# Performance work log

Hardware: AMD Instinct MI355X
Metric: run time of the kernel (lower is better)

## Reference

```python
import jax, jax.numpy as jnp
import numpy as np

B, L, C = 4, 2048, 512
D_STATE, D_CONV, EXPAND = 16, 4, 2
D_INNER = EXPAND * C
DT_RANK = C // 16  # mamba_ssm 'auto' dt_rank


def setup_inputs() -> dict:
    key = jax.random.key(0)
    ks = jax.random.split(key, 12)
    s = 0.02
    p = {}
    p["x"] = jax.random.normal(ks[0], (B, L, C), jnp.float32)
    p["gamma1"] = jnp.ones((C,), jnp.float32)
    p["beta1"] = jnp.zeros((C,), jnp.float32)
    # leading dim 2 = (forward mamba, backward mamba)
    p["W_in"] = jax.random.normal(ks[1], (2, 2 * D_INNER, C), jnp.float32) * s
    p["conv_w"] = jax.random.normal(ks[2], (2, D_INNER, D_CONV), jnp.float32) * s
    p["conv_b"] = jnp.zeros((2, D_INNER), jnp.float32)
    p["W_xproj"] = jax.random.normal(ks[3], (2, DT_RANK + 2 * D_STATE, D_INNER), jnp.float32) * s
    p["W_dt"] = jax.random.normal(ks[4], (2, D_INNER, DT_RANK), jnp.float32) * s
    p["b_dt"] = jax.random.normal(ks[5], (2, D_INNER), jnp.float32) * s
    p["A_log"] = jnp.tile(jnp.log(jnp.arange(1, D_STATE + 1, dtype=jnp.float32))[None, None, :], (2, D_INNER, 1))
    p["Dp"] = jnp.ones((2, D_INNER), jnp.float32)
    p["W_out"] = jax.random.normal(ks[6], (2, C, D_INNER), jnp.float32) * s
    p["gamma2"] = jnp.ones((C,), jnp.float32)
    p["beta2"] = jnp.zeros((C,), jnp.float32)
    p["W1"] = jax.random.normal(ks[7], (4 * C, C), jnp.float32) * s
    p["b1"] = jnp.zeros((4 * C,), jnp.float32)
    p["W2"] = jax.random.normal(ks[8], (C, 4 * C), jnp.float32) * s
    p["b2"] = jnp.zeros((C,), jnp.float32)
    return p


def layer_norm(x, g, b, eps=1e-5):
    mu = x.mean(-1, keepdims=True)
    var = ((x - mu) ** 2).mean(-1, keepdims=True)
    return (x - mu) * jax.lax.rsqrt(var + eps) * g + b


def mamba_one(x, W_in, conv_w, conv_b, W_xproj, W_dt, b_dt, A_log, Dv, W_out):
    # x: [B, L, C] -> [B, L, C]; faithful to mamba_ssm Mamba (in_proj no bias,
    # depthwise causal conv1d with bias, x_proj no bias, dt_proj with bias, out_proj no bias)
    u, z = jnp.split(x @ W_in.T, 2, axis=-1)          # [B,L,d_inner] each
    uc = jnp.pad(u.transpose(0, 2, 1), ((0, 0), (0, 0), (D_CONV - 1, 0)))  # causal pad
    uc = jax.lax.conv_general_dilated(uc, conv_w[:, None, :], (1,), 'VALID',
                                      feature_group_count=D_INNER)
    u = jax.nn.silu((uc + conv_b[None, :, None]).transpose(0, 2, 1))       # [B,L,d_inner]
    x_dbl = u @ W_xproj.T                              # [B,L,dt_rank+2*d_state]
    dt = jax.nn.softplus(x_dbl[..., :DT_RANK] @ W_dt.T + b_dt)             # [B,L,d_inner]
    Bm = x_dbl[..., DT_RANK:DT_RANK + D_STATE]         # [B,L,d_state]
    Cm = x_dbl[..., DT_RANK + D_STATE:]                # [B,L,d_state]
    A = -jnp.exp(A_log)                                # [d_inner,d_state]

    def step(h, ins):
        dt_t, B_t, C_t, u_t = ins                      # [B,d],[B,s],[B,s],[B,d]
        h = jnp.exp(dt_t[..., None] * A) * h + (dt_t * u_t)[..., None] * B_t[:, None, :]
        return h, jnp.einsum('bds,bs->bd', h, C_t)

    h0 = jnp.zeros((x.shape[0], D_INNER, D_STATE), x.dtype)
    xs = (dt.transpose(1, 0, 2), Bm.transpose(1, 0, 2), Cm.transpose(1, 0, 2), u.transpose(1, 0, 2))
    _, ys = jax.lax.scan(step, h0, xs)                 # ys: [L,B,d_inner]
    y = ys.transpose(1, 0, 2) + u * Dv
    y = y * jax.nn.silu(z)
    return y @ W_out.T


def reference(x, gamma1, beta1, W_in, conv_w, conv_b, W_xproj, W_dt, b_dt,
              A_log, Dp, W_out, gamma2, beta2, W1, b1, W2, b2):
    xn = layer_norm(x, gamma1, beta1)
    x2 = jnp.stack([xn, jnp.flip(xn, axis=1)])         # [2,B,L,C]
    ys = jax.vmap(mamba_one)(x2, W_in, conv_w, conv_b, W_xproj, W_dt, b_dt, A_log, Dp, W_out)
    y = (ys[0] + jnp.flip(ys[1], axis=1)) * 0.5
    x = x + y                                          # residual (dropout=0)
    h = jax.nn.gelu(layer_norm(x, gamma2, beta2) @ W1.T + b1, approximate=False)
    return x + (h @ W2.T + b2)
```

## Files before the change

### kernel.cpp

```cpp
#include <hip/hip_runtime.h>
#include <math.h>

#define B_ 4
#define L_ 2048
#define C_ 512
#define DI 1024
#define DS 16
#define NTOK 8192
#define SLICE ((long)NTOK * DI)
#define T_ 64
#define NC_ 32
#define SDT_LD 264

typedef __attribute__((ext_vector_type(4))) float  f32x4;
typedef __attribute__((ext_vector_type(4))) short  s16x4;
typedef __attribute__((ext_vector_type(8))) short  s16x8;
typedef __attribute__((ext_vector_type(8))) __bf16 bf16x8;

#define LOG2E 1.4426950408889634f
#define LN2   0.69314718055994531f

__device__ __forceinline__ float bf2f(short s) {
  return __uint_as_float(((unsigned)(unsigned short)s) << 16);
}
__device__ __forceinline__ short f2bf(float f) {
  return __builtin_bit_cast(short, (__bf16)f);
}
__device__ __forceinline__ f32x4 mfma16(s16x8 a, s16x8 b, f32x4 c) {
  return __builtin_amdgcn_mfma_f32_16x16x32_bf16(
      __builtin_bit_cast(bf16x8, a), __builtin_bit_cast(bf16x8, b), c, 0, 0, 0);
}
__device__ __forceinline__ float fast_sigmoid(float z) {
  return __builtin_amdgcn_rcpf(1.f + __builtin_amdgcn_exp2f(-LOG2E * z));
}
__device__ __forceinline__ float fast_softplus(float t) {
  return (t > 15.f) ? t
    : LN2 * __builtin_amdgcn_logf(1.f + __builtin_amdgcn_exp2f(LOG2E * t));
}

__global__ __launch_bounds__(256) void castw_all(
    const float* __restrict__ s0, short* __restrict__ d0,
    const float* __restrict__ s1, short* __restrict__ d1,
    const float* __restrict__ s2, short* __restrict__ d2,
    const float* __restrict__ s3, short* __restrict__ d3,
    const float* __restrict__ s4, short* __restrict__ d4,
    const float* __restrict__ s5, short* __restrict__ d5)
{
  int b = blockIdx.x;
  const float* s; short* d; int off;
  if      (b < 2048) { s = s0; d = d0; off = b; }
  else if (b < 2176) { s = s1; d = d1; off = b - 2048; }
  else if (b < 2240) { s = s2; d = d2; off = b - 2176; }
  else if (b < 3264) { s = s3; d = d3; off = b - 2240; }
  else if (b < 4288) { s = s4; d = d4; off = b - 3264; }
  else               { s = s5; d = d5; off = b - 4288; }
  int i = (off * 256 + threadIdx.x) * 4;
  f32x4 v = *(const f32x4*)(s + i);
  s16x4 o;
#pragma unroll
  for (int k = 0; k < 4; ++k) o[k] = f2bf(v[k]);
  *(s16x4*)(d + i) = o;
}

__global__ __launch_bounds__(256) void ln1_kernel(
    const float* __restrict__ x, const float* __restrict__ g,
    const float* __restrict__ bt, short* __restrict__ out)
{
  int tok  = blockIdx.x * 4 + (threadIdx.x >> 6);
  int lane = threadIdx.x & 63;
  const float* row = x + (long)tok * C_ + lane * 8;
  f32x4 a0 = *(const f32x4*)row, a1 = *(const f32x4*)(row + 4);
  float s = 0.f, q = 0.f;
#pragma unroll
  for (int i = 0; i < 4; ++i) { s += a0[i] + a1[i]; q += a0[i]*a0[i] + a1[i]*a1[i]; }
#pragma unroll
  for (int o = 1; o < 64; o <<= 1) { s += __shfl_xor(s, o); q += __shfl_xor(q, o); }
  float mu = s * (1.f / C_);
  float rs = rsqrtf(q * (1.f / C_) - mu * mu + 1e-5f);
  f32x4 g0 = *(const f32x4*)(g + lane*8), g1 = *(const f32x4*)(g + lane*8 + 4);
  f32x4 b0 = *(const f32x4*)(bt + lane*8), b1 = *(const f32x4*)(bt + lane*8 + 4);
  s16x8 o8;
#pragma unroll
  for (int i = 0; i < 4; ++i) {
    o8[i]     = f2bf((a0[i] - mu) * rs * g0[i] + b0[i]);
    o8[4 + i] = f2bf((a1[i] - mu) * rs * g1[i] + b1[i]);
  }
  *(s16x8*)(out + (long)tok * C_ + lane * 8) = o8;
}

__global__ __launch_bounds__(256) void combine_ln2_kernel(
    const float* __restrict__ x, const short* __restrict__ yob,
    const float* __restrict__ g, const float* __restrict__ bt,
    float* __restrict__ xmid, short* __restrict__ xln)
{
  int tok  = blockIdx.x * 4 + (threadIdx.x >> 6);
  int lane = threadIdx.x & 63;
  long base = (long)tok * C_ + lane * 8;
  f32x4 a0 = *(const f32x4*)(x + base),  a1 = *(const f32x4*)(x + base + 4);
  s16x8 p8 = *(const s16x8*)(yob + base);
  s16x8 q8 = *(const s16x8*)(yob + (long)NTOK * C_ + base);
#pragma unroll
  for (int i = 0; i < 4; ++i) {
    a0[i] += 0.5f * (bf2f(p8[i]) + bf2f(q8[i]));
    a1[i] += 0.5f * (bf2f(p8[4 + i]) + bf2f(q8[4 + i]));
  }
  *(f32x4*)(xmid + base) = a0;
  *(f32x4*)(xmid + base + 4) = a1;
  float s = 0.f, q = 0.f;
#pragma unroll
  for (int i = 0; i < 4; ++i) { s += a0[i] + a1[i]; q += a0[i]*a0[i] + a1[i]*a1[i]; }
#pragma unroll
  for (int o = 1; o < 64; o <<= 1) { s += __shfl_xor(s, o); q += __shfl_xor(q, o); }
  float mu = s * (1.f / C_);
  float rs = rsqrtf(q * (1.f / C_) - mu * mu + 1e-5f);
  f32x4 g0 = *(const f32x4*)(g + lane*8), g1 = *(const f32x4*)(g + lane*8 + 4);
  f32x4 b0 = *(const f32x4*)(bt + lane*8), b1 = *(const f32x4*)(bt + lane*8 + 4);
  s16x8 o8;
#pragma unroll
  for (int i = 0; i < 4; ++i) {
    o8[i]     = f2bf((a0[i] - mu) * rs * g0[i] + b0[i]);
    o8[4 + i] = f2bf((a1[i] - mu) * rs * g1[i] + b1[i]);
  }
  *(s16x8*)(xln + (long)tok * C_ + lane * 8) = o8;
}

__global__ __launch_bounds__(256) void conv_silu_kernel(
    const short* __restrict__ ubuf, const float* __restrict__ cw,
    const float* __restrict__ cb, short* __restrict__ ucv)
{
  int ch = blockIdx.x * 256 + threadIdx.x;
  int tc = blockIdx.y;
  int db = blockIdx.z;
  int d = db >> 2, b = db & 3;
  const short* U = ubuf + ((long)d * NTOK + (long)b * L_) * DI + ch;
  short* O = ucv + ((long)d * NTOK + (long)b * L_) * DI + ch;
  f32x4 w4 = *(const f32x4*)(cw + ((long)d * DI + ch) * 4);
  float bias = cb[d * DI + ch];
  int t0 = tc * 128;
  if (d == 0) {
    float h3 = (t0 >= 3) ? bf2f(U[(long)(t0 - 3) * DI]) : 0.f;
    float h2 = (t0 >= 2) ? bf2f(U[(long)(t0 - 2) * DI]) : 0.f;
    float h1 = (t0 >= 1) ? bf2f(U[(long)(t0 - 1) * DI]) : 0.f;
    for (int t = t0; t < t0 + 128; ++t) {
      float cur = bf2f(U[(long)t * DI]);
      float v = w4[0]*h3 + w4[1]*h2 + w4[2]*h1 + w4[3]*cur + bias;
      v = v * fast_sigmoid(v);
      O[(long)t * DI] = f2bf(v);
      h3 = h2; h2 = h1; h1 = cur;
    }
  } else {
    float a0v = bf2f(U[(long)t0 * DI]);
    float a1v = (t0 + 1 < L_) ? bf2f(U[(long)(t0 + 1) * DI]) : 0.f;
    float a2v = (t0 + 2 < L_) ? bf2f(U[(long)(t0 + 2) * DI]) : 0.f;
    for (int t = t0; t < t0 + 128; ++t) {
      float a3v = (t + 3 < L_) ? bf2f(U[(long)(t + 3) * DI]) : 0.f;
      float v = w4[3]*a0v + w4[2]*a1v + w4[1]*a2v + w4[0]*a3v + bias;
      v = v * fast_sigmoid(v);
      O[(long)t * DI] = f2bf(v);
      a0v = a1v; a1v = a2v; a2v = a3v;
    }
  }
}

template <int PASS, int DIR>
__device__ __forceinline__ void scan_body(
    const short* __restrict__ up, const short* __restrict__ zp,
    short* __restrict__ yp, const float* __restrict__ sBC,
    const short* __restrict__ sdt, int tid,
    const float* A2, float* h, float Dv, float& S)
{
#pragma unroll
  for (int ib = 0; ib < T_ / 8; ++ib) {
    const int t0 = DIR ? (T_ - 8 - ib * 8) : ib * 8;
    float u8[8], z8[8];
#pragma unroll
    for (int j = 0; j < 8; ++j) {
      long o = (long)(t0 + j) * DI;
      u8[j] = bf2f(up[o]);
      if (PASS == 1) z8[j] = bf2f(zp[o]);
    }
    short y8[8];
#pragma unroll
    for (int jj = 0; jj < 8; ++jj) {
      const int j = DIR ? (7 - jj) : jj;
      float dtv = bf2f(sdt[(t0 + j) * SDT_LD + tid]);
      float uv  = u8[j];
      float wv = dtv * uv;
      const float* bc = &sBC[(t0 + j) * (PASS ? 32 : 16)];
      float p = 0.f;
#pragma unroll
      for (int s = 0; s < 16; ++s) {
        float e = __builtin_amdgcn_exp2f(dtv * A2[s]);
        h[s] = e * h[s] + wv * bc[s];
        if (PASS == 1) p += h[s] * bc[16 + s];
      }
      if (PASS == 0) {
        S += dtv;
      } else {
        float z = z8[j];
        y8[j] = f2bf((p + uv * Dv) * (z * fast_sigmoid(z)));
      }
    }
    if (PASS == 1) {
#pragma unroll
      for (int j = 0; j < 8; ++j) yp[(long)(t0 + j) * DI] = y8[j];
    }
  }
}

template <int PASS>
__global__ __launch_bounds__(256) void scan_pass(
    const short* __restrict__ dtr, const short* __restrict__ wdt,
    const float* __restrict__ bdt,
    const short* __restrict__ ucv, const float* __restrict__ xdbl,
    const short* __restrict__ zbuf,
    const float* __restrict__ Alog, const float* __restrict__ Dp,
    float* __restrict__ hbuf, float* __restrict__ Sbuf, short* __restrict__ ybuf)
{
  __shared__ float sBC[T_ * 32];
  __shared__ short sdt[T_ * SDT_LD];
  const int tid  = threadIdx.x;
  const int lane = tid & 63;
  const int w    = tid >> 6;
  const int ch   = blockIdx.x * 256 + tid;
  const int c    = blockIdx.y;
  const int db   = blockIdx.z;
  const int d    = db >> 2, b = db & 3;
  const long n0  = (long)b * L_ + (long)c * T_;
  const float* xrow = xdbl + ((long)d * NTOK + n0) * 64 + 32;
  if (PASS == 0) {
    int r = tid >> 2, cc4 = (tid & 3) * 4;
    *(f32x4*)&sBC[r * 16 + cc4] = *(const f32x4*)(xrow + (long)r * 64 + cc4);
  } else {
    int r = tid >> 2, cc8 = (tid & 3) * 8;
    *(f32x4*)&sBC[r * 32 + cc8]     = *(const f32x4*)(xrow + (long)r * 64 + cc8);
    *(f32x4*)&sBC[r * 32 + cc8 + 4] = *(const f32x4*)(xrow + (long)r * 64 + cc8 + 4);
  }
  {
    const short* dtrp = dtr + ((long)d * NTOK + n0) * 32;
    const short* wp   = wdt + ((long)d * DI + blockIdx.x * 256) * 32;
    s16x8 af[4], bfr[4];
#pragma unroll
    for (int mi = 0; mi < 4; ++mi)
      af[mi] = *(const s16x8*)(dtrp + (mi * 16 + (lane & 15)) * 32 + (lane >> 4) * 8);
#pragma unroll
    for (int ni = 0; ni < 4; ++ni)
      bfr[ni] = *(const s16x8*)(wp + (w * 64 + ni * 16 + (lane & 15)) * 32 + (lane >> 4) * 8);
    float bv[4];
#pragma unroll
    for (int ni = 0; ni < 4; ++ni)
      bv[ni] = bdt[d * DI + blockIdx.x * 256 + w * 64 + ni * 16 + (lane & 15)];
#pragma unroll
    for (int mi = 0; mi < 4; ++mi) {
#pragma unroll
      for (int ni = 0; ni < 4; ++ni) {
        f32x4 acc = {0.f, 0.f, 0.f, 0.f};
        acc = mfma16(af[mi], bfr[ni], acc);
#pragma unroll
        for (int j = 0; j < 4; ++j) {
          float sp = fast_softplus(acc[j] + bv[ni]);
          sdt[(mi * 16 + (lane >> 4) * 4 + j) * SDT_LD + w * 64 + ni * 16 + (lane & 15)]
            = f2bf(sp);
        }
      }
    }
  }
  __syncthreads();
  float A2[16];
  {
    const float* Ap = Alog + ((long)d * DI + ch) * DS;
#pragma unroll
    for (int s = 0; s < 16; ++s) A2[s] = -expf(Ap[s]) * LOG2E;
  }
  const long base = ((long)d * NTOK + n0) * DI + ch;
  const short* up  = ucv + base;
  const short* zp  = zbuf + base;
  short* yp = ybuf + base;
  const long hb = (((long)db * NC_ + c) * DI + ch) * 16;
  float h[16];
  float Dv = 0.f;
  if (PASS == 1) {
#pragma unroll
    for (int s = 0; s < 16; s += 4) *(f32x4*)&h[s] = *(const f32x4*)&hbuf[hb + s];
    Dv = Dp[d * DI + ch];
  } else {
#pragma unroll
    for (int s = 0; s < 16; ++s) h[s] = 0.f;
  }
  float S = 0.f;
  if (d == 0) scan_body<PASS, 0>(up, zp, yp, sBC, sdt, tid, A2, h, Dv, S);
  else        scan_body<PASS, 1>(up, zp, yp, sBC, sdt, tid, A2, h, Dv, S);
  if (PASS == 0) {
#pragma unroll
    for (int s = 0; s < 16; s += 4) *(f32x4*)&hbuf[hb + s] = *(const f32x4*)&h[s];
    Sbuf[((long)db * NC_ + c) * DI + ch] = S;
  }
}

__global__ __launch_bounds__(256) void scan_combine(
    const float* __restrict__ Alog, float* __restrict__ hbuf,
    const float* __restrict__ Sbuf)
{
  int tid = threadIdx.x;
  int ch = (blockIdx.x & 3) * 256 + tid;
  int db = blockIdx.x >> 2;
  int d = db >> 2;
  float A2[16];
  const float* Ap = Alog + ((long)d * DI + ch) * DS;
#pragma unroll
  for (int s = 0; s < 16; ++s) A2[s] = -expf(Ap[s]) * LOG2E;
  float h[16];
#pragma unroll
  for (int s = 0; s < 16; ++s) h[s] = 0.f;
  for (int cc = 0; cc < NC_; ++cc) {
    int c = (d == 1) ? (NC_ - 1 - cc) : cc;
    long hb = (((long)db * NC_ + c) * DI + ch) * 16;
    float S = Sbuf[((long)db * NC_ + c) * DI + ch];
    float he[16];
#pragma unroll
    for (int s = 0; s < 16; s += 4) *(f32x4*)&he[s] = *(const f32x4*)&hbuf[hb + s];
#pragma unroll
    for (int s = 0; s < 16; s += 4) *(f32x4*)&hbuf[hb + s] = *(const f32x4*)&h[s];
#pragma unroll
    for (int s = 0; s < 16; ++s) h[s] = __builtin_amdgcn_exp2f(A2[s] * S) * h[s] + he[s];
  }
}

template <int EPI, int BM, int BN>
__global__ __launch_bounds__(256) void gemm_m97(
    const short* __restrict__ X, long sX,
    const short* __restrict__ Wb, long sW,
    const float* __restrict__ bias, long sBias,
    float* __restrict__ outF, long sOutF,
    short* __restrict__ outB,
    const float* __restrict__ res,
    short* __restrict__ outB2,
    int K, int N)
{
  constexpr int NWN = BN / 64;
  constexpr int NWM = 4 / NWN;
  constexpr int MI  = BM / (16 * NWM);
  __shared__ short sA[BM * 32];
  __shared__ short sB[BN * 32];
  const int tid  = threadIdx.x;
  const int lane = tid & 63;
  const int w    = tid >> 6;
  const int wm   = (NWN == 2) ? (w >> 1) : w;
  const int wn   = (NWN == 2) ? (w & 1) : 0;
  const int d    = blockIdx.z;
  const int m0   = blockIdx.x * BM;
  const int n0   = blockIdx.y * BN;
  const short* Xp = X + (long)d * sX + (long)m0 * K;
  const short* Wp = Wb + (long)d * sW + (long)n0 * K;

  f32x4 acc[MI][4];
#pragma unroll
  for (int i = 0; i < MI; ++i)
#pragma unroll
    for (int j = 0; j < 4; ++j) acc[i][j] = (f32x4){0.f, 0.f, 0.f, 0.f};

  const int lrow = lane >> 2;
  const int lkg  = lane & 3;

  for (int k0 = 0; k0 < K; k0 += 32) {
#pragma unroll
    for (int j = 0; j < BM / 64; ++j) {
      int row = w * 16 + j * 64 + lrow;
      int kgs = lkg ^ ((row >> 1) & 3);
      __builtin_amdgcn_global_load_lds(
        (const __attribute__((address_space(1))) unsigned*)(Xp + (long)row * K + k0 + kgs * 8),
        (__attribute__((address_space(3))) unsigned*)(sA + (w * 16 + j * 64) * 32),
        16, 0, 0);
    }
#pragma unroll
    for (int j = 0; j < BN / 64; ++j) {
      int row = w * 16 + j * 64 + lrow;
      int kgs = lkg ^ ((row >> 1) & 3);
      __builtin_amdgcn_global_load_lds(
        (const __attribute__((address_space(1))) unsigned*)(Wp + (long)row * K + k0 + kgs * 8),
        (__attribute__((address_space(3))) unsigned*)(sB + (w * 16 + j * 64) * 32),
        16, 0, 0);
    }
    __syncthreads();
    s16x8 af[MI], bfr[4];
#pragma unroll
    for (int mi = 0; mi < MI; ++mi) {
      int row = wm * (MI * 16) + mi * 16 + (lane & 15);
      int kg = (lane >> 4) ^ ((row >> 1) & 3);
      af[mi] = *(const s16x8*)((const char*)sA + row * 64 + kg * 16);
    }
#pragma unroll
    for (int ni = 0; ni < 4; ++ni) {
      int row = wn * 64 + ni * 16 + (lane & 15);
      int kg = (lane >> 4) ^ ((row >> 1) & 3);
      bfr[ni] = *(const s16x8*)((const char*)sB + row * 64 + kg * 16);
    }
#pragma unroll
    for (int mi = 0; mi < MI; ++mi)
#pragma unroll
      for (int ni = 0; ni < 4; ++ni)
        acc[mi][ni] = mfma16(af[mi], bfr[ni], acc[mi][ni]);
    __syncthreads();
  }

  const int col0 = lane & 15;
  const int rsub = (lane >> 4) * 4;
#pragma unroll
  for (int mi = 0; mi < MI; ++mi) {
    int row = m0 + wm * (MI * 16) + mi * 16 + rsub;
#pragma unroll
    for (int ni = 0; ni < 4; ++ni) {
      int col = n0 + wn * 64 + ni * 16 + col0;
#pragma unroll
      for (int j = 0; j < 4; ++j) {
        float v = acc[mi][ni][j];
        int r = row + j;
        if constexpr (EPI == 0) {
          outF[(long)d * sOutF + (long)r * N + col] = v;
        } else if constexpr (EPI == 1) {
          int d2 = col >> 11, cc = col & 2047;
          long o = ((long)d2 * NTOK + r) * DI;
          if (cc < DI) outB[o + cc] = f2bf(v);
          else         outB2[o + cc - DI] = f2bf(v);
        } else if constexpr (EPI == 3) {
          float t = v + bias[col];
          float u3 = t * (1.f + 0.044715f * t * t);
          float sg = __builtin_amdgcn_rcpf(1.f + __builtin_amdgcn_exp2f(-2.3022083f * u3));
          outB[(long)r * N + col] = f2bf(t * sg);
        } else if constexpr (EPI == 4) {
          outF[(long)r * N + col] = v + bias[col] + res[(long)r * N + col];
        } else if constexpr (EPI == 5) {
          if (col < 32) outB[((long)d * NTOK + r) * 32 + col] = f2bf(v);
          else          outF[((long)d * NTOK + r) * 64 + col] = v;
        } else if constexpr (EPI == 6) {
          outB[((long)d * NTOK + r) * N + col] = f2bf(v);
        }
      }
    }
  }
}

extern "C" void kernel_launch(void* const* d_in, const int* in_sizes, int n_in,
                              void* d_out, int out_size, void* d_ws, size_t ws_size,
                              hipStream_t stream) {
  const float* x      = (const float*)d_in[0];
  const float* gamma1 = (const float*)d_in[1];
  const float* beta1  = (const float*)d_in[2];
  const float* W_in   = (const float*)d_in[3];
  const float* conv_w = (const float*)d_in[4];
  const float* conv_b = (const float*)d_in[5];
  const float* W_xprj = (const float*)d_in[6];
  const float* W_dt   = (const float*)d_in[7];
  const float* b_dt   = (const float*)d_in[8];
  const float* A_log  = (const float*)d_in[9];
  const float* Dp     = (const float*)d_in[10];
  const float* W_out  = (const float*)d_in[11];
  const float* gamma2 = (const float*)d_in[12];
  const float* beta2  = (const float*)d_in[13];
  const float* W1     = (const float*)d_in[14];
  const float* b1     = (const float*)d_in[15];
  const float* W2     = (const float*)d_in[16];
  const float* b2     = (const float*)d_in[17];
  float* out = (float*)d_out;

  char* ws = (char*)d_ws;
  short* wb_in  = (short*)(ws);
  short* wb_xp  = (short*)(ws + (4L << 20));
  short* wb_dt  = (short*)(ws + (4L << 20) + (256L << 10));
  short* wb_out = (short*)(ws + (4L << 20) + (384L << 10));
  short* wb_w1  = (short*)(ws + (6L << 20) + (384L << 10));
  short* wb_w2  = (short*)(ws + (8L << 20) + (384L << 10));
  short* xnbf = (short*)(ws + (12L << 20));
  short* ubuf = (short*)(ws + (20L << 20));
  short* zbuf = (short*)(ws + (52L << 20));
  short* ucv  = (short*)(ws + (84L << 20));
  short* Hbuf = (short*)(ws + (116L << 20));
  float* xdbl = (float*)(ws + (148L << 20));
  short* dtr  = (short*)(ws + (152L << 20));
  float* hbuf = (float*)(ws + (153L << 20));
  float* Sbuf = (float*)(ws + (169L << 20));
  float* xmid = (float*)(ws + (170L << 20));
  short* ybf  = zbuf;
  short* xln  = xnbf;

  castw_all<<<5312, 256, 0, stream>>>(W_in, wb_in, W_xprj, wb_xp, W_dt, wb_dt,
                                      W_out, wb_out, W1, wb_w1, W2, wb_w2);
  ln1_kernel<<<NTOK / 4, 256, 0, stream>>>(x, gamma1, beta1, xnbf);
  gemm_m97<1, 128, 128><<<dim3(64, 32, 1), 256, 0, stream>>>(
      xnbf, 0, wb_in, 0, nullptr, 0, nullptr, 0, ubuf, nullptr, zbuf, C_, 4096);
  conv_silu_kernel<<<dim3(4, 16, 8), 256, 0, stream>>>(ubuf, conv_w, conv_b, ucv);
  gemm_m97<5, 64, 64><<<dim3(128, 1, 2), 256, 0, stream>>>(
      ucv, SLICE, wb_xp, 64L * DI, nullptr, 0, xdbl, 0, dtr, nullptr, nullptr, DI, 64);
  scan_pass<0><<<dim3(4, NC_, 8), 256, 0, stream>>>(dtr, wb_dt, b_dt, ucv, xdbl, zbuf, A_log, Dp, hbuf, Sbuf, ucv);
  scan_combine<<<32, 256, 0, stream>>>(A_log, hbuf, Sbuf);
  scan_pass<1><<<dim3(4, NC_, 8), 256, 0, stream>>>(dtr, wb_dt, b_dt, ucv, xdbl, zbuf, A_log, Dp, hbuf, Sbuf, ucv);
  gemm_m97<6, 64, 128><<<dim3(128, 4, 2), 256, 0, stream>>>(
      ucv, SLICE, wb_out, (long)C_ * DI, nullptr, 0, nullptr, 0, ybf,
      nullptr, nullptr, DI, C_);
  combine_ln2_kernel<<<NTOK / 4, 256, 0, stream>>>(x, ybf, gamma2, beta2, xmid, xln);
  gemm_m97<3, 128, 128><<<dim3(64, 16, 1), 256, 0, stream>>>(
      xln, 0, wb_w1, 0, b1, 0, nullptr, 0, Hbuf, nullptr, nullptr, C_, 2048);
  gemm_m97<4, 64, 128><<<dim3(128, 4, 1), 256, 0, stream>>>(
      Hbuf, 0, wb_w2, 0, b2, 0, out, 0, nullptr, xmid, nullptr, 2048, C_);
}
```

Measured before the change: 399.5 us.

## Transpose and swizzle dt tile in LDS, vectorize B/C loads, raise occupancy

Stores the softplus(dt) tile channel-major with an XOR swizzle, so each thread fetches 8 timesteps with one 16-byte LDS read instead of 8 scalar reads. The GEMM epilogue now writes 4 timesteps as one packed vector store. B/C coefficients are read as float4 vectors. The sBC array is sized per pass, and launch bounds ask for 4 blocks per CU, which may cap register use and cause spills.

```diff
diff --git a/kernel.cpp b/kernel.cpp
--- a/kernel.cpp
+++ b/kernel.cpp
@@ -10,7 +10,6 @@
 #define SLICE ((long)NTOK * DI)
 #define T_ 64
 #define NC_ 32
-#define SDT_LD 264
 
 typedef __attribute__((ext_vector_type(4))) float  f32x4;
 typedef __attribute__((ext_vector_type(4))) short  s16x4;
@@ -36,6 +35,9 @@
 __device__ __forceinline__ float fast_softplus(float t) {
   return (t > 15.f) ? t
     : LN2 * __builtin_amdgcn_logf(1.f + __builtin_amdgcn_exp2f(LOG2E * t));
+}
+__device__ __forceinline__ int sdt_off(int ch, int t) {
+  return ch * 64 + ((t & 0x38) ^ ((ch & 7) << 3)) + (t & 7);
 }
 
 __global__ __launch_bounds__(256) void castw_all(
@@ -172,6 +174,7 @@
 #pragma unroll
   for (int ib = 0; ib < T_ / 8; ++ib) {
     const int t0 = DIR ? (T_ - 8 - ib * 8) : ib * 8;
+    const s16x8 dt8 = *(const s16x8*)&sdt[tid * 64 + ((t0 & 0x38) ^ ((tid & 7) << 3))];
     float u8[8], z8[8];
 #pragma unroll
     for (int j = 0; j < 8; ++j) {
@@ -183,16 +186,23 @@
 #pragma unroll
     for (int jj = 0; jj < 8; ++jj) {
       const int j = DIR ? (7 - jj) : jj;
-      float dtv = bf2f(sdt[(t0 + j) * SDT_LD + tid]);
+      float dtv = bf2f(dt8[j]);
       float uv  = u8[j];
       float wv = dtv * uv;
       const float* bc = &sBC[(t0 + j) * (PASS ? 32 : 16)];
       float p = 0.f;
 #pragma unroll
-      for (int s = 0; s < 16; ++s) {
-        float e = __builtin_amdgcn_exp2f(dtv * A2[s]);
-        h[s] = e * h[s] + wv * bc[s];
-        if (PASS == 1) p += h[s] * bc[16 + s];
+      for (int g = 0; g < 4; ++g) {
+        f32x4 b4 = *(const f32x4*)&bc[g * 4];
+        f32x4 c4;
+        if (PASS == 1) c4 = *(const f32x4*)&bc[16 + g * 4];
+#pragma unroll
+        for (int k = 0; k < 4; ++k) {
+          const int s = g * 4 + k;
+          float e = __builtin_amdgcn_exp2f(dtv * A2[s]);
+          h[s] = e * h[s] + wv * b4[k];
+          if (PASS == 1) p += h[s] * c4[k];
+        }
       }
       if (PASS == 0) {
         S += dtv;
@@ -209,7 +219,7 @@
 }
 
 template <int PASS>
-__global__ __launch_bounds__(256) void scan_pass(
+__global__ __launch_bounds__(256, 4) void scan_pass(
     const short* __restrict__ dtr, const short* __restrict__ wdt,
     const float* __restrict__ bdt,
     const short* __restrict__ ucv, const float* __restrict__ xdbl,
@@ -217,8 +227,8 @@
     const float* __restrict__ Alog, const float* __restrict__ Dp,
     float* __restrict__ hbuf, float* __restrict__ Sbuf, short* __restrict__ ybuf)
 {
-  __shared__ float sBC[T_ * 32];
-  __shared__ short sdt[T_ * SDT_LD];
+  __shared__ float sBC[T_ * (PASS ? 32 : 16)];
+  __shared__ short sdt[256 * 64];
   const int tid  = threadIdx.x;
   const int lane = tid & 63;
   const int w    = tid >> 6;
@@ -252,16 +262,17 @@
       bv[ni] = bdt[d * DI + blockIdx.x * 256 + w * 64 + ni * 16 + (lane & 15)];
 #pragma unroll
     for (int mi = 0; mi < 4; ++mi) {
+      const int tb = mi * 16 + (lane >> 4) * 4;
 #pragma unroll
       for (int ni = 0; ni < 4; ++ni) {
         f32x4 acc = {0.f, 0.f, 0.f, 0.f};
         acc = mfma16(af[mi], bfr[ni], acc);
-#pragma unroll
-        for (int j = 0; j < 4; ++j) {
-          float sp = fast_softplus(acc[j] + bv[ni]);
-          sdt[(mi * 16 + (lane >> 4) * 4 + j) * SDT_LD + w * 64 + ni * 16 + (lane & 15)]
-            = f2bf(sp);
-        }
+        const int col = w * 64 + ni * 16 + (lane & 15);
+        s16x4 o;
+#pragma unroll
+        for (int j = 0; j < 4; ++j)
+          o[j] = f2bf(fast_softplus(acc[j] + bv[ni]));
+        *(s16x4*)&sdt[sdt_off(col, tb)] = o;
       }
     }
   }
```

After: 1.328 ms. +232.4%, slower.
